# Performance work log

Hardware: AMD Instinct MI355X
Metric: run time of the kernel (lower is better)

## Reference

```python
import jax, jax.numpy as jnp
import numpy as np

N, IN_DIM, OUT_DIM, HEADS = 8192, 256, 128, 2


def setup_inputs() -> dict:
    key = jax.random.key(0)
    k1, k2, k3, k4, k5 = jax.random.split(key, 5)
    features = jax.random.normal(k1, (N, IN_DIM), dtype=jnp.float32)
    adjacency = jax.random.randint(k2, (N, N), 0, 2, dtype=jnp.int32)
    # nn.Linear(input_dim, output_dim*heads, bias=False): weight [out, in]
    W = jax.random.normal(k3, (OUT_DIM * HEADS, IN_DIM), dtype=jnp.float32) * 0.05
    attn_src = jax.random.normal(k4, (HEADS, OUT_DIM), dtype=jnp.float32) * 0.05
    attn_dst = jax.random.normal(k5, (HEADS, OUT_DIM), dtype=jnp.float32) * 0.05
    return {"features": features, "adjacency": adjacency, "W": W,
            "attn_src": attn_src, "attn_dst": attn_dst}


def reference(features, adjacency, W, attn_src, attn_dst):
    n = features.shape[0]
    # transformed: [N, H, F]
    transformed = (features @ W.T).reshape(n, HEADS, OUT_DIM)
    src_scores = jnp.einsum('nhf,hf->nh', transformed, attn_src)  # [N, H]
    dst_scores = jnp.einsum('nhf,hf->nh', transformed, attn_dst)  # [N, H]
    # logits: [N_src, N_dst, H]
    logits = jax.nn.leaky_relu(src_scores[:, None, :] + dst_scores[None, :, :],
                               negative_slope=0.2)
    mask = adjacency > 0  # [N, N]
    logits = jnp.where(mask[:, :, None], logits, -jnp.inf)
    attention = jax.nn.softmax(logits, axis=1)  # softmax over dst dim (dim=1)
    attention = jnp.nan_to_num(attention, nan=0.0, posinf=0.0, neginf=0.0)
    aggregated = jnp.einsum('ijh,jhf->ihf', attention, transformed)  # [N, H, F]
    return aggregated.mean(axis=1)  # [N, F]
```

## Files before the change

kernel.cpp:

```cpp
#include <hip/hip_runtime.h>
#include <stdint.h>
#include <stddef.h>

#define NN 8192
#define KD 256
#define CD 256
#define FD 128
#define BI 64
#define BJ 64
#define LOG2E 1.44269504f

typedef __attribute__((ext_vector_type(4))) float f32x4;
typedef __attribute__((ext_vector_type(2))) float f32x2;
typedef __attribute__((ext_vector_type(8))) short b16x8;

__device__ __forceinline__ unsigned int cvtpk(float lo, float hi) {
    unsigned int r;
    asm("v_cvt_pk_bf16_f32 %0, %1, %2" : "=v"(r) : "v"(lo), "v"(hi));
    return r;
}

__device__ __forceinline__ float exp2raw(float x) {
    float r;
    asm("v_exp_f32 %0, %1\n\ts_nop 0" : "=v"(r) : "v"(x));
    return r;
}

__device__ __forceinline__ void async16(const void* g, void* l) {
    __builtin_amdgcn_global_load_lds(
        (const __attribute__((address_space(1))) unsigned int*)g,
        (__attribute__((address_space(3))) unsigned int*)l, 16, 0, 0);
}

__global__ __launch_bounds__(256) void k_transform(
    const float* __restrict__ feat, const float* __restrict__ W,
    const float* __restrict__ asrc, const float* __restrict__ adst,
    unsigned short* __restrict__ Tt, float* __restrict__ s, float* __restrict__ d)
{
    __shared__ unsigned short a_lds[32 * 32];
    __shared__ unsigned short b_lds[256 * 32];
    __shared__ unsigned short tr_lds[256 * 40];
    __shared__ float sc_lds[4][32];
    __shared__ float dc_lds[4][32];

    const int t = threadIdx.x;
    const int wave = t >> 6, lane = t & 63;
    const int l15 = lane & 15, quad = lane >> 4;
    const int n0 = blockIdx.x * 32;

    f32x4 acc[2][4] = {};
    for (int kc = 0; kc < 8; ++kc) {
        const int k0 = kc * 32;
        __syncthreads();
        if (t < 128) {
            const int ai = t >> 2, ag = t & 3;
            const float* src = feat + (size_t)(n0 + ai) * KD + k0 + ag * 8;
            const float4 v0 = *(const float4*)src;
            const float4 v1 = *(const float4*)(src + 4);
            union { unsigned int u[4]; b16x8 v; } pk;
            pk.u[0] = cvtpk(v0.x, v0.y); pk.u[1] = cvtpk(v0.z, v0.w);
            pk.u[2] = cvtpk(v1.x, v1.y); pk.u[3] = cvtpk(v1.z, v1.w);
            const int slot = ag ^ ((ai >> 1) & 3);
            *(b16x8*)&a_lds[ai * 32 + slot * 8] = pk.v;
        }
        for (int p = 0; p < 4; ++p) {
            const int G = p * 256 + t;
            const int c = G >> 2, g = G & 3;
            const float* src = W + (size_t)c * KD + k0 + g * 8;
            const float4 v0 = *(const float4*)src;
            const float4 v1 = *(const float4*)(src + 4);
            union { unsigned int u[4]; b16x8 v; } pk;
            pk.u[0] = cvtpk(v0.x, v0.y); pk.u[1] = cvtpk(v0.z, v0.w);
            pk.u[2] = cvtpk(v1.x, v1.y); pk.u[3] = cvtpk(v1.z, v1.w);
            const int slot = g ^ ((c >> 1) & 3);
            *(b16x8*)&b_lds[c * 32 + slot * 8] = pk.v;
        }
        __syncthreads();
        b16x8 af[2], bfr[4];
        for (int mt = 0; mt < 2; ++mt) {
            const int m = mt * 16 + l15;
            af[mt] = *(const b16x8*)&a_lds[m * 32 + (quad ^ ((m >> 1) & 3)) * 8];
        }
        for (int nt = 0; nt < 4; ++nt) {
            const int c = wave * 64 + nt * 16 + l15;
            bfr[nt] = *(const b16x8*)&b_lds[c * 32 + (quad ^ ((c >> 1) & 3)) * 8];
        }
        for (int mt = 0; mt < 2; ++mt)
            for (int nt = 0; nt < 4; ++nt)
                acc[mt][nt] = __builtin_amdgcn_mfma_f32_16x16x32_bf16(
                    af[mt], bfr[nt], acc[mt][nt], 0, 0, 0);
    }

    float aS[4], aD[4];
    for (int nt = 0; nt < 4; ++nt) {
        const int c = wave * 64 + nt * 16 + l15;
        aS[nt] = asrc[c]; aD[nt] = adst[c];
    }
    for (int mt = 0; mt < 2; ++mt)
        for (int r = 0; r < 4; ++r) {
            float vs = 0.f, vd = 0.f;
            for (int nt = 0; nt < 4; ++nt) {
                const float x = acc[mt][nt][r];
                vs += x * aS[nt]; vd += x * aD[nt];
            }
            vs += __shfl_xor(vs, 1); vd += __shfl_xor(vd, 1);
            vs += __shfl_xor(vs, 2); vd += __shfl_xor(vd, 2);
            vs += __shfl_xor(vs, 4); vd += __shfl_xor(vd, 4);
            vs += __shfl_xor(vs, 8); vd += __shfl_xor(vd, 8);
            if (l15 == 0) {
                const int nl = mt * 16 + quad * 4 + r;
                sc_lds[wave][nl] = vs; dc_lds[wave][nl] = vd;
            }
        }
    for (int mt = 0; mt < 2; ++mt)
        for (int nt = 0; nt < 4; ++nt) {
            const int c = wave * 64 + nt * 16 + l15;
            const int n = mt * 16 + quad * 4;
            *(unsigned int*)&tr_lds[c * 40 + n] =
                cvtpk(acc[mt][nt][0], acc[mt][nt][1]);
            *(unsigned int*)&tr_lds[c * 40 + n + 2] =
                cvtpk(acc[mt][nt][2], acc[mt][nt][3]);
        }
    __syncthreads();
    if (t < 64) {
        const int n = t >> 1, h = t & 1;
        s[(size_t)(n0 + n) * 2 + h] = (sc_lds[h * 2][n] + sc_lds[h * 2 + 1][n]) * LOG2E;
        d[(size_t)(n0 + n) * 2 + h] = (dc_lds[h * 2][n] + dc_lds[h * 2 + 1][n]) * LOG2E;
    }
    for (int p = 0; p < 4; ++p) {
        const int idx = p * 256 + t;
        const int c = idx >> 2, g = idx & 3;
        *(b16x8*)(Tt + (size_t)c * NN + n0 + g * 8) = *(const b16x8*)&tr_lds[c * 40 + g * 8];
    }
}

__global__ __launch_bounds__(512, 4) void k_gat(
    const int* __restrict__ adj, const unsigned short* __restrict__ Tt,
    const float* __restrict__ s, const float* __restrict__ d,
    float* __restrict__ num_part,
    float* __restrict__ den_part,
    int jchunk)
{
    __shared__ unsigned short tt_lds[2][CD * BJ];
    __shared__ unsigned short w_lds[2 * BI * BJ];

    const int t = threadIdx.x;
    const int w = t >> 6, lane = t & 63;
    const int l15 = lane & 15, quad = lane >> 4;
    const int h  = (w >> 2) & 1;
    const int fh = (w >> 1) & 1;
    const int rh = w & 1;
    const int i0 = blockIdx.x * BI;
    const int chunk = blockIdx.y;
    const int jbase = chunk * jchunk;

    const int wi = t >> 3;
    const int j8 = t & 7;
    const int gi = i0 + wi;
    const f32x2 s01 = *(const f32x2*)(s + (size_t)gi * 2);
    const int cbase = h * 128 + fh * 64;

    f32x4 acc[2][4] = {};
    float den0 = 0.f, den1 = 0.f;
    const int njt = jchunk / BJ;

    const int* arow = adj + (size_t)gi * NN + j8 * 8;
    const float* drow = d + (size_t)j8 * 16;
    const int c0 = w * 8 + (lane >> 3);
    const int g0 = (lane & 7) ^ (c0 & 7);
    const unsigned short* tsrc0 = Tt + (size_t)c0 * NN + g0 * 8;
    const int toff0 = w * 1024;
    const int slot = (j8 ^ (wi & 7)) << 3;
    unsigned short* wp0 = &w_lds[(0 * BI + wi) * BJ + slot];
    const int m0 = rh * 32 + l15;
    const int afb = (h * BI + m0) * BJ;
    const int bfb = (cbase + l15) * BJ;
    const int X[2] = {((0 * 4 + quad) ^ (l15 & 7)) << 3,
                      ((1 * 4 + quad) ^ (l15 & 7)) << 3};

    #pragma unroll
    for (int p = 0; p < 4; ++p)
        async16(tsrc0 + (size_t)p * 64 * NN + jbase,
                (char*)&tt_lds[0][0] + toff0 + p * 8192);
    int4 aA0 = *(const int4*)(arow + jbase);
    int4 aA1 = *(const int4*)(arow + jbase + 4);
    const float4* dpp = (const float4*)(drow + 2 * jbase);
    float4 dA0 = dpp[0], dA1 = dpp[1], dA2 = dpp[2], dA3 = dpp[3];
    int4 aB0, aB1; float4 dB0, dB1, dB2, dB3;

    auto body = [&](int jt, int buf,
                    int4& ca0, int4& ca1, float4& cd0, float4& cd1, float4& cd2, float4& cd3,
                    int4& na0, int4& na1, float4& nd0, float4& nd1, float4& nd2, float4& nd3) {
        const int j0 = jbase + jt * BJ;
        __builtin_amdgcn_s_barrier();
        const int jn = (jt + 1 < njt) ? j0 + BJ : j0;
        #pragma unroll
        for (int p = 0; p < 4; ++p)
            async16(tsrc0 + (size_t)p * 64 * NN + jn,
                    (char*)&tt_lds[buf ^ 1][0] + toff0 + p * 8192);
        na0 = *(const int4*)(arow + jn);
        na1 = *(const int4*)(arow + jn + 4);
        { const float4* dnp = (const float4*)(drow + 2 * jn);
          nd0 = dnp[0]; nd1 = dnp[1]; nd2 = dnp[2]; nd3 = dnp[3]; }
        union { float4 v[4]; f32x2 p[8]; } dv;
        dv.v[0] = cd0; dv.v[1] = cd1; dv.v[2] = cd2; dv.v[3] = cd3;
        const int am[8] = {ca0.x, ca0.y, ca0.z, ca0.w, ca1.x, ca1.y, ca1.z, ca1.w};
        f32x2 ef[8];
        f32x2 dp = {0.f, 0.f};
        #pragma unroll
        for (int e = 0; e < 8; ++e) {
            const f32x2 x = s01 + dv.p[e];
            const f32x2 xm = __builtin_elementwise_max(x, 0.2f * x);
            const float r0 = exp2raw(xm.x), r1 = exp2raw(xm.y);
            const f32x2 em = {am[e] != 0 ? r0 : 0.f, am[e] != 0 ? r1 : 0.f};
            ef[e] = em; dp += em;
        }
        den0 += dp.x; den1 += dp.y;
        union { unsigned int u[4]; b16x8 v; } w0, w1;
        #pragma unroll
        for (int q = 0; q < 4; ++q) {
            w0.u[q] = cvtpk(ef[2 * q].x, ef[2 * q + 1].x);
            w1.u[q] = cvtpk(ef[2 * q].y, ef[2 * q + 1].y);
        }
        *(b16x8*)wp0 = w0.v;
        *(b16x8*)(wp0 + BI * BJ) = w1.v;
        asm volatile("s_waitcnt vmcnt(10) lgkmcnt(0)" ::: "memory");
        __builtin_amdgcn_s_barrier();
        __builtin_amdgcn_sched_barrier(0);
        __builtin_amdgcn_s_setprio(1);
        #pragma unroll
        for (int ks = 0; ks < 2; ++ks) {
            b16x8 af[2], bf[4];
            #pragma unroll
            for (int mt = 0; mt < 2; ++mt)
                af[mt] = *(const b16x8*)&w_lds[afb + mt * 1024 + X[ks]];
            #pragma unroll
            for (int nt = 0; nt < 4; ++nt)
                bf[nt] = *(const b16x8*)&tt_lds[buf][bfb + nt * 1024 + X[ks]];
            #pragma unroll
            for (int mt = 0; mt < 2; ++mt)
                #pragma unroll
                for (int nt = 0; nt < 4; ++nt)
                    acc[mt][nt] = __builtin_amdgcn_mfma_f32_16x16x32_bf16(
                        af[mt], bf[nt], acc[mt][nt], 0, 0, 0);
        }
        __builtin_amdgcn_s_setprio(0);
    };

    for (int jt = 0; jt < njt; jt += 2) {
        body(jt,     0, aA0, aA1, dA0, dA1, dA2, dA3, aB0, aB1, dB0, dB1, dB2, dB3);
        body(jt + 1, 1, aB0, aB1, dB0, dB1, dB2, dB3, aA0, aA1, dA0, dA1, dA2, dA3);
    }
    asm volatile("s_waitcnt vmcnt(0)" ::: "memory");
    den0 += __shfl_xor(den0, 1); den0 += __shfl_xor(den0, 2); den0 += __shfl_xor(den0, 4);
    den1 += __shfl_xor(den1, 1); den1 += __shfl_xor(den1, 2); den1 += __shfl_xor(den1, 4);
    if (j8 == 0) {
        den_part[((size_t)chunk * 2 + 0) * NN + gi] = den0;
        den_part[((size_t)chunk * 2 + 1) * NN + gi] = den1;
    }
    float* np_ = num_part + (size_t)chunk * NN * CD;
    for (int mt = 0; mt < 2; ++mt)
        for (int nt = 0; nt < 4; ++nt)
            for (int r = 0; r < 4; ++r) {
                const int n = i0 + rh * 32 + mt * 16 + quad * 4 + r;
                const int c = cbase + nt * 16 + l15;
                np_[(size_t)n * CD + c] = acc[mt][nt][r];
            }
}

__global__ __launch_bounds__(256) void k_combine(
    const float* __restrict__ num_part, const float* __restrict__ den_part,
    float* __restrict__ out, int jsplit)
{
    const int idx = blockIdx.x * 256 + threadIdx.x;
    const int n = idx >> 7, f = idx & 127;
    const size_t row = (size_t)n * CD;
    float n0 = 0.f, n1 = 0.f, d0 = 0.f, d1 = 0.f;
    for (int c = 0; c < jsplit; ++c) {
        const size_t base = (size_t)c * NN * CD;
        n0 += num_part[base + row + f];
        n1 += num_part[base + row + 128 + f];
        d0 += den_part[((size_t)c * 2 + 0) * NN + n];
        d1 += den_part[((size_t)c * 2 + 1) * NN + n];
    }
    const float r0 = d0 != 0.f ? n0 / d0 : 0.f;
    const float r1 = d1 != 0.f ? n1 / d1 : 0.f;
    out[idx] = 0.5f * (r0 + r1);
}

extern "C" void kernel_launch(void* const* d_in, const int* in_sizes, int n_in,
                              void* d_out, int out_size, void* d_ws, size_t ws_size,
                              hipStream_t stream) {
    const float* feat = (const float*)d_in[0];
    const int*   adj  = (const int*)d_in[1];
    const float* W    = (const float*)d_in[2];
    const float* asrc = (const float*)d_in[3];
    const float* adst = (const float*)d_in[4];
    float* out = (float*)d_out;

    const int jsplit = (ws_size >= ((size_t)40 << 20)) ? 4 : 2;
    const int jchunk = NN / jsplit;

    char* ws = (char*)d_ws;
    unsigned short* Tt = (unsigned short*)ws;
    float* s    = (float*)(ws + ((size_t)4 << 20));
    float* dsc  = (float*)(ws + ((size_t)4 << 20) + (64 << 10));
    float* den  = (float*)(ws + ((size_t)4 << 20) + (128 << 10));
    float* nump = (float*)(ws + ((size_t)8 << 20));

    k_transform<<<256, 256, 0, stream>>>(feat, W, asrc, adst, Tt, s, dsc);
    k_gat<<<dim3(NN / BI, jsplit), 512, 0, stream>>>(adj, Tt, s, dsc, nump, den, jchunk);
    k_combine<<<NN * FD / 256, 256, 0, stream>>>(nump, den, out, jsplit);
}
```

Baseline: 435.6 us.

## Split GAT attention kernel per head to halve LDS and double occupancy

New measurement: 498.5 us. 14.4% more time.

```diff
diff --git a/kernel.cpp b/kernel.cpp
--- a/kernel.cpp
+++ b/kernel.cpp
@@ -124,8 +124,8 @@
     __syncthreads();
     if (t < 64) {
         const int n = t >> 1, h = t & 1;
-        s[(size_t)(n0 + n) * 2 + h] = (sc_lds[h * 2][n] + sc_lds[h * 2 + 1][n]) * LOG2E;
-        d[(size_t)(n0 + n) * 2 + h] = (dc_lds[h * 2][n] + dc_lds[h * 2 + 1][n]) * LOG2E;
+        s[(size_t)h * NN + n0 + n] = (sc_lds[h * 2][n] + sc_lds[h * 2 + 1][n]) * LOG2E;
+        d[(size_t)h * NN + n0 + n] = (dc_lds[h * 2][n] + dc_lds[h * 2 + 1][n]) * LOG2E;
     }
     for (int p = 0; p < 4; ++p) {
         const int idx = p * 256 + t;
@@ -134,113 +134,106 @@
     }
 }
 
-__global__ __launch_bounds__(512, 4) void k_gat(
+__global__ __launch_bounds__(512, 8) void k_gat(
     const int* __restrict__ adj, const unsigned short* __restrict__ Tt,
     const float* __restrict__ s, const float* __restrict__ d,
     float* __restrict__ num_part,
     float* __restrict__ den_part,
     int jchunk)
 {
-    __shared__ unsigned short tt_lds[2][CD * BJ];
-    __shared__ unsigned short w_lds[2 * BI * BJ];
+    __shared__ unsigned short tt_lds[2][128 * BJ];
+    __shared__ unsigned short w_lds[BI * BJ];
 
     const int t = threadIdx.x;
     const int w = t >> 6, lane = t & 63;
     const int l15 = lane & 15, quad = lane >> 4;
-    const int h  = (w >> 2) & 1;
-    const int fh = (w >> 1) & 1;
-    const int rh = w & 1;
-    const int i0 = blockIdx.x * BI;
+    const int rh = w >> 2;
+    const int ch = w & 3;
+    const int bx = blockIdx.x;
+    const int i0 = (bx >> 1) * BI;
+    const int h  = bx & 1;
     const int chunk = blockIdx.y;
     const int jbase = chunk * jchunk;
 
     const int wi = t >> 3;
     const int j8 = t & 7;
     const int gi = i0 + wi;
-    const f32x2 s01 = *(const f32x2*)(s + (size_t)gi * 2);
-    const int cbase = h * 128 + fh * 64;
-
-    f32x4 acc[2][4] = {};
-    float den0 = 0.f, den1 = 0.f;
+    const float sh = s[(size_t)h * NN + gi];
     const int njt = jchunk / BJ;
 
+    f32x4 acc[2][2] = {};
+    float den = 0.f;
+
     const int* arow = adj + (size_t)gi * NN + j8 * 8;
-    const float* drow = d + (size_t)j8 * 16;
+    const float* drow = d + (size_t)h * NN + j8 * 8;
     const int c0 = w * 8 + (lane >> 3);
     const int g0 = (lane & 7) ^ (c0 & 7);
-    const unsigned short* tsrc0 = Tt + (size_t)c0 * NN + g0 * 8;
+    const unsigned short* tsrc0 = Tt + (size_t)(h * 128 + c0) * NN + g0 * 8;
     const int toff0 = w * 1024;
     const int slot = (j8 ^ (wi & 7)) << 3;
-    unsigned short* wp0 = &w_lds[(0 * BI + wi) * BJ + slot];
-    const int m0 = rh * 32 + l15;
-    const int afb = (h * BI + m0) * BJ;
-    const int bfb = (cbase + l15) * BJ;
+    unsigned short* wp0 = &w_lds[wi * BJ + slot];
+    const int afb = (rh * 32 + l15) * BJ;
+    const int bfb = (ch * 32 + l15) * BJ;
     const int X[2] = {((0 * 4 + quad) ^ (l15 & 7)) << 3,
                       ((1 * 4 + quad) ^ (l15 & 7)) << 3};
 
     #pragma unroll
-    for (int p = 0; p < 4; ++p)
+    for (int p = 0; p < 2; ++p)
         async16(tsrc0 + (size_t)p * 64 * NN + jbase,
                 (char*)&tt_lds[0][0] + toff0 + p * 8192);
     int4 aA0 = *(const int4*)(arow + jbase);
     int4 aA1 = *(const int4*)(arow + jbase + 4);
-    const float4* dpp = (const float4*)(drow + 2 * jbase);
-    float4 dA0 = dpp[0], dA1 = dpp[1], dA2 = dpp[2], dA3 = dpp[3];
-    int4 aB0, aB1; float4 dB0, dB1, dB2, dB3;
+    const float4* dpp = (const float4*)(drow + jbase);
+    float4 dA0 = dpp[0], dA1 = dpp[1];
+    int4 aB0, aB1; float4 dB0, dB1;
 
     auto body = [&](int jt, int buf,
-                    int4& ca0, int4& ca1, float4& cd0, float4& cd1, float4& cd2, float4& cd3,
-                    int4& na0, int4& na1, float4& nd0, float4& nd1, float4& nd2, float4& nd3) {
+                    int4& ca0, int4& ca1, float4& cd0, float4& cd1,
+                    int4& na0, int4& na1, float4& nd0, float4& nd1) {
         const int j0 = jbase + jt * BJ;
         __builtin_amdgcn_s_barrier();
         const int jn = (jt + 1 < njt) ? j0 + BJ : j0;
         #pragma unroll
-        for (int p = 0; p < 4; ++p)
+        for (int p = 0; p < 2; ++p)
             async16(tsrc0 + (size_t)p * 64 * NN + jn,
                     (char*)&tt_lds[buf ^ 1][0] + toff0 + p * 8192);
         na0 = *(const int4*)(arow + jn);
         na1 = *(const int4*)(arow + jn + 4);
-        { const float4* dnp = (const float4*)(drow + 2 * jn);
-          nd0 = dnp[0]; nd1 = dnp[1]; nd2 = dnp[2]; nd3 = dnp[3]; }
-        union { float4 v[4]; f32x2 p[8]; } dv;
-        dv.v[0] = cd0; dv.v[1] = cd1; dv.v[2] = cd2; dv.v[3] = cd3;
-        const int am[8] = {ca0.x, ca0.y, ca0.z, ca0.w, ca1.x, ca1.y, ca1.z, ca1.w};
-        f32x2 ef[8];
-        f32x2 dp = {0.f, 0.f};
+        { const float4* dnp = (const float4*)(drow + jn);
+          nd0 = dnp[0]; nd1 = dnp[1]; }
+        const int   am[8] = {ca0.x, ca0.y, ca0.z, ca0.w, ca1.x, ca1.y, ca1.z, ca1.w};
+        const float dvf[8] = {cd0.x, cd0.y, cd0.z, cd0.w, cd1.x, cd1.y, cd1.z, cd1.w};
+        float ef[8], dp = 0.f;
         #pragma unroll
         for (int e = 0; e < 8; ++e) {
-            const f32x2 x = s01 + dv.p[e];
-            const f32x2 xm = __builtin_elementwise_max(x, 0.2f * x);
-            const float r0 = exp2raw(xm.x), r1 = exp2raw(xm.y);
-            const f32x2 em = {am[e] != 0 ? r0 : 0.f, am[e] != 0 ? r1 : 0.f};
-            ef[e] = em; dp += em;
-        }
-        den0 += dp.x; den1 += dp.y;
-        union { unsigned int u[4]; b16x8 v; } w0, w1;
+            float x = sh + dvf[e];
+            x = fmaxf(x, 0.2f * x);
+            ef[e] = am[e] != 0 ? exp2raw(x) : 0.f;
+            dp += ef[e];
+        }
+        den += dp;
+        union { unsigned int u[4]; b16x8 v; } w0;
         #pragma unroll
-        for (int q = 0; q < 4; ++q) {
-            w0.u[q] = cvtpk(ef[2 * q].x, ef[2 * q + 1].x);
-            w1.u[q] = cvtpk(ef[2 * q].y, ef[2 * q + 1].y);
-        }
+        for (int q = 0; q < 4; ++q)
+            w0.u[q] = cvtpk(ef[2 * q], ef[2 * q + 1]);
         *(b16x8*)wp0 = w0.v;
-        *(b16x8*)(wp0 + BI * BJ) = w1.v;
-        asm volatile("s_waitcnt vmcnt(10) lgkmcnt(0)" ::: "memory");
+        asm volatile("s_waitcnt vmcnt(6) lgkmcnt(0)" ::: "memory");
         __builtin_amdgcn_s_barrier();
         __builtin_amdgcn_sched_barrier(0);
         __builtin_amdgcn_s_setprio(1);
         #pragma unroll
         for (int ks = 0; ks < 2; ++ks) {
-            b16x8 af[2], bf[4];
+            b16x8 af[2], bf[2];
             #pragma unroll
             for (int mt = 0; mt < 2; ++mt)
                 af[mt] = *(const b16x8*)&w_lds[afb + mt * 1024 + X[ks]];
             #pragma unroll
-            for (int nt = 0; nt < 4; ++nt)
+            for (int nt = 0; nt < 2; ++nt)
                 bf[nt] = *(const b16x8*)&tt_lds[buf][bfb + nt * 1024 + X[ks]];
             #pragma unroll
             for (int mt = 0; mt < 2; ++mt)
                 #pragma unroll
-                for (int nt = 0; nt < 4; ++nt)
+                for (int nt = 0; nt < 2; ++nt)
                     acc[mt][nt] = __builtin_amdgcn_mfma_f32_16x16x32_bf16(
                         af[mt], bf[nt], acc[mt][nt], 0, 0, 0);
         }
@@ -248,22 +241,19 @@
     };
 
     for (int jt = 0; jt < njt; jt += 2) {
-        body(jt,     0, aA0, aA1, dA0, dA1, dA2, dA3, aB0, aB1, dB0, dB1, dB2, dB3);
-        body(jt + 1, 1, aB0, aB1, dB0, dB1, dB2, dB3, aA0, aA1, dA0, dA1, dA2, dA3);
+        body(jt,     0, aA0, aA1, dA0, dA1, aB0, aB1, dB0, dB1);
+        body(jt + 1, 1, aB0, aB1, dB0, dB1, aA0, aA1, dA0, dA1);
     }
     asm volatile("s_waitcnt vmcnt(0)" ::: "memory");
-    den0 += __shfl_xor(den0, 1); den0 += __shfl_xor(den0, 2); den0 += __shfl_xor(den0, 4);
-    den1 += __shfl_xor(den1, 1); den1 += __shfl_xor(den1, 2); den1 += __shfl_xor(den1, 4);
-    if (j8 == 0) {
-        den_part[((size_t)chunk * 2 + 0) * NN + gi] = den0;
-        den_part[((size_t)chunk * 2 + 1) * NN + gi] = den1;
-    }
+    den += __shfl_xor(den, 1); den += __shfl_xor(den, 2); den += __shfl_xor(den, 4);
+    if (j8 == 0)
+        den_part[((size_t)chunk * 2 + h) * NN + gi] = den;
     float* np_ = num_part + (size_t)chunk * NN * CD;
     for (int mt = 0; mt < 2; ++mt)
-        for (int nt = 0; nt < 4; ++nt)
+        for (int nt = 0; nt < 2; ++nt)
             for (int r = 0; r < 4; ++r) {
                 const int n = i0 + rh * 32 + mt * 16 + quad * 4 + r;
-                const int c = cbase + nt * 16 + l15;
+                const int c = h * 128 + ch * 32 + nt * 16 + l15;
                 np_[(size_t)n * CD + c] = acc[mt][nt][r];
             }
 }
@@ -309,6 +299,6 @@
     float* nump = (float*)(ws + ((size_t)8 << 20));
 
     k_transform<<<256, 256, 0, stream>>>(feat, W, asrc, adst, Tt, s, dsc);
-    k_gat<<<dim3(NN / BI, jsplit), 512, 0, stream>>>(adj, Tt, s, dsc, nump, den, jchunk);
+    k_gat<<<dim3((NN / BI) * 2, jsplit), 512, 0, stream>>>(adj, Tt, s, dsc, nump, den, jchunk);
     k_combine<<<NN * FD / 256, 256, 0, stream>>>(nump, den, out, jsplit);
 }
```

## Pre-pack adjacency into bitmasks before the attention kernel

Applied to the files above, without the earlier changes.

New measurement: 470.5 us. +8.0%, slower.

```diff
diff --git a/kernel.cpp b/kernel.cpp
--- a/kernel.cpp
+++ b/kernel.cpp
@@ -30,6 +30,21 @@
     __builtin_amdgcn_global_load_lds(
         (const __attribute__((address_space(1))) unsigned int*)g,
         (__attribute__((address_space(3))) unsigned int*)l, 16, 0, 0);
+}
+
+__global__ __launch_bounds__(256) void k_pack(
+    const int* __restrict__ adj, unsigned long long* __restrict__ bits)
+{
+    const int lane = threadIdx.x & 63;
+    const int gw = blockIdx.x * 4 + (threadIdx.x >> 6);
+    const int nwaves = gridDim.x * 4;
+    const int total = NN * (NN / 64);
+    for (int idx = gw; idx < total; idx += nwaves) {
+        const int row = idx >> 7, w64 = idx & 127;
+        const int v = adj[(size_t)row * NN + w64 * 64 + lane];
+        const unsigned long long m = __ballot(v != 0);
+        if (lane == 0) bits[idx] = m;
+    }
 }
 
 __global__ __launch_bounds__(256) void k_transform(
@@ -135,7 +150,7 @@
 }
 
 __global__ __launch_bounds__(512, 4) void k_gat(
-    const int* __restrict__ adj, const unsigned short* __restrict__ Tt,
+    const unsigned long long* __restrict__ bits, const unsigned short* __restrict__ Tt,
     const float* __restrict__ s, const float* __restrict__ d,
     float* __restrict__ num_part,
     float* __restrict__ den_part,
@@ -164,7 +179,7 @@
     float den0 = 0.f, den1 = 0.f;
     const int njt = jchunk / BJ;
 
-    const int* arow = adj + (size_t)gi * NN + j8 * 8;
+    const unsigned long long* brow = bits + (size_t)gi * (NN / 64);
     const float* drow = d + (size_t)j8 * 16;
     const int c0 = w * 8 + (lane >> 3);
     const int g0 = (lane & 7) ^ (c0 & 7);
@@ -177,20 +192,20 @@
     const int bfb = (cbase + l15) * BJ;
     const int X[2] = {((0 * 4 + quad) ^ (l15 & 7)) << 3,
                       ((1 * 4 + quad) ^ (l15 & 7)) << 3};
+    const int sh8 = j8 * 8;
 
     #pragma unroll
     for (int p = 0; p < 4; ++p)
         async16(tsrc0 + (size_t)p * 64 * NN + jbase,
                 (char*)&tt_lds[0][0] + toff0 + p * 8192);
-    int4 aA0 = *(const int4*)(arow + jbase);
-    int4 aA1 = *(const int4*)(arow + jbase + 4);
+    unsigned long long bA = brow[jbase >> 6];
     const float4* dpp = (const float4*)(drow + 2 * jbase);
     float4 dA0 = dpp[0], dA1 = dpp[1], dA2 = dpp[2], dA3 = dpp[3];
-    int4 aB0, aB1; float4 dB0, dB1, dB2, dB3;
+    unsigned long long bB; float4 dB0, dB1, dB2, dB3;
 
     auto body = [&](int jt, int buf,
-                    int4& ca0, int4& ca1, float4& cd0, float4& cd1, float4& cd2, float4& cd3,
-                    int4& na0, int4& na1, float4& nd0, float4& nd1, float4& nd2, float4& nd3) {
+                    unsigned long long& cb, float4& cd0, float4& cd1, float4& cd2, float4& cd3,
+                    unsigned long long& nb, float4& nd0, float4& nd1, float4& nd2, float4& nd3) {
         const int j0 = jbase + jt * BJ;
         __builtin_amdgcn_s_barrier();
         const int jn = (jt + 1 < njt) ? j0 + BJ : j0;
@@ -198,13 +213,12 @@
         for (int p = 0; p < 4; ++p)
             async16(tsrc0 + (size_t)p * 64 * NN + jn,
                     (char*)&tt_lds[buf ^ 1][0] + toff0 + p * 8192);
-        na0 = *(const int4*)(arow + jn);
-        na1 = *(const int4*)(arow + jn + 4);
+        nb = brow[jn >> 6];
         { const float4* dnp = (const float4*)(drow + 2 * jn);
           nd0 = dnp[0]; nd1 = dnp[1]; nd2 = dnp[2]; nd3 = dnp[3]; }
         union { float4 v[4]; f32x2 p[8]; } dv;
         dv.v[0] = cd0; dv.v[1] = cd1; dv.v[2] = cd2; dv.v[3] = cd3;
-        const int am[8] = {ca0.x, ca0.y, ca0.z, ca0.w, ca1.x, ca1.y, ca1.z, ca1.w};
+        const unsigned int byte = (unsigned int)(cb >> sh8) & 0xffu;
         f32x2 ef[8];
         f32x2 dp = {0.f, 0.f};
         #pragma unroll
@@ -212,7 +226,8 @@
             const f32x2 x = s01 + dv.p[e];
             const f32x2 xm = __builtin_elementwise_max(x, 0.2f * x);
             const float r0 = exp2raw(xm.x), r1 = exp2raw(xm.y);
-            const f32x2 em = {am[e] != 0 ? r0 : 0.f, am[e] != 0 ? r1 : 0.f};
+            const bool on = (byte >> e) & 1u;
+            const f32x2 em = {on ? r0 : 0.f, on ? r1 : 0.f};
             ef[e] = em; dp += em;
         }
         den0 += dp.x; den1 += dp.y;
@@ -224,7 +239,7 @@
         }
         *(b16x8*)wp0 = w0.v;
         *(b16x8*)(wp0 + BI * BJ) = w1.v;
-        asm volatile("s_waitcnt vmcnt(10) lgkmcnt(0)" ::: "memory");
+        asm volatile("s_waitcnt vmcnt(9) lgkmcnt(0)" ::: "memory");
         __builtin_amdgcn_s_barrier();
         __builtin_amdgcn_sched_barrier(0);
         __builtin_amdgcn_s_setprio(1);
@@ -248,8 +263,8 @@
     };
 
     for (int jt = 0; jt < njt; jt += 2) {
-        body(jt,     0, aA0, aA1, dA0, dA1, dA2, dA3, aB0, aB1, dB0, dB1, dB2, dB3);
-        body(jt + 1, 1, aB0, aB1, dB0, dB1, dB2, dB3, aA0, aA1, dA0, dA1, dA2, dA3);
+        body(jt,     0, bA, dA0, dA1, dA2, dA3, bB, dB0, dB1, dB2, dB3);
+        body(jt + 1, 1, bB, dB0, dB1, dB2, dB3, bA, dA0, dA1, dA2, dA3);
     }
     asm volatile("s_waitcnt vmcnt(0)" ::: "memory");
     den0 += __shfl_xor(den0, 1); den0 += __shfl_xor(den0, 2); den0 += __shfl_xor(den0, 4);
@@ -298,7 +313,7 @@
     const float* adst = (const float*)d_in[4];
     float* out = (float*)d_out;
 
-    const int jsplit = (ws_size >= ((size_t)40 << 20)) ? 4 : 2;
+    const int jsplit = (ws_size >= ((size_t)48 << 20)) ? 4 : 2;
     const int jchunk = NN / jsplit;
 
     char* ws = (char*)d_ws;
@@ -307,8 +322,10 @@
     float* dsc  = (float*)(ws + ((size_t)4 << 20) + (64 << 10));
     float* den  = (float*)(ws + ((size_t)4 << 20) + (128 << 10));
     float* nump = (float*)(ws + ((size_t)8 << 20));
-
+    unsigned long long* bits = (unsigned long long*)(ws + ((size_t)40 << 20));
+
+    k_pack<<<2048, 256, 0, stream>>>(adj, bits);
     k_transform<<<256, 256, 0, stream>>>(feat, W, asrc, adst, Tt, s, dsc);
-    k_gat<<<dim3(NN / BI, jsplit), 512, 0, stream>>>(adj, Tt, s, dsc, nump, den, jchunk);
+    k_gat<<<dim3(NN / BI, jsplit), 512, 0, stream>>>(bits, Tt, s, dsc, nump, den, jchunk);
     k_combine<<<NN * FD / 256, 256, 0, stream>>>(nump, den, out, jsplit);
 }
```
